# Optimization experiments

Measured on AMD Instinct MI355X. Metric: run time of the kernel, lower is better.

Reference implementation:

```python
import math
import jax, jax.numpy as jnp
import numpy as np

H = 12
D = 64  # head dim

def _heads(x):
    # [b, n, h*d] -> [b, h, n, d]
    b, n, _ = x.shape
    return x.reshape(b, n, H, D).transpose(0, 2, 1, 3)

def setup_inputs() -> dict:
    key = jax.random.key(0)
    ks = jax.random.split(key, 9)
    hs = 768
    s = 1.0 / math.sqrt(hs)
    return {
        "query_states": jax.random.normal(ks[0], (8, 1024, hs), jnp.float32),
        "key_states": jax.random.normal(ks[1], (8, 1024, hs), jnp.float32),
        "Wd": jax.random.normal(ks[2], (hs, hs), jnp.float32) * s,
        "Wq": jax.random.normal(ks[3], (hs, hs), jnp.float32) * s,
        "bq": jax.random.normal(ks[4], (hs,), jnp.float32) * 0.01,
        "Wk": jax.random.normal(ks[5], (hs, hs), jnp.float32) * s,
        "bk": jax.random.normal(ks[6], (hs,), jnp.float32) * 0.01,
        "Wv": jax.random.normal(ks[7], (hs, hs), jnp.float32) * s,
        "bv": jax.random.normal(ks[8], (hs,), jnp.float32) * 0.01,
    }

def reference(query_states, key_states, Wd, Wq, bq, Wk, bk, Wv, bv):
    # projections (torch Linear: x @ W.T + b)
    qd = _heads(query_states @ Wd.T)          # [b,h,n,d]
    kd = _heads(key_states @ Wd.T)
    q = _heads(query_states @ Wq.T + bq)
    k = _heads(key_states @ Wk.T + bk)
    v = _heads(key_states @ Wv.T + bv)
    # -0.5 * cdist(qd, kd)^2 = -0.5*(|qd|^2 + |kd|^2) + qd@kd^T
    qd_sq = jnp.sum(qd * qd, axis=-1)          # [b,h,n]
    kd_sq = jnp.sum(kd * kd, axis=-1)          # [b,h,m]
    quad = (qd @ jnp.swapaxes(kd, -1, -2)
            - 0.5 * qd_sq[..., :, None]
            - 0.5 * kd_sq[..., None, :])       # [b,h,n,m]
    lin = q @ jnp.swapaxes(k, -1, -2)          # [b,h,n,m]
    scores = (quad + lin) / math.sqrt(D)
    probs = jax.nn.softmax(scores, axis=-1)
    ctx = probs @ v                            # [b,h,n,d]
    b, _, n, _ = ctx.shape
    return ctx.transpose(0, 2, 1, 3).reshape(b, n, H * D)
```

## Files before the change

kernel.cpp:

```cpp
#include <hip/hip_runtime.h>
#include <stdint.h>

typedef __attribute__((ext_vector_type(8))) short short8;
typedef __attribute__((ext_vector_type(4))) short short4v;
typedef __attribute__((ext_vector_type(4))) float f32x4;
typedef __attribute__((ext_vector_type(16))) float f32x16;
typedef __attribute__((ext_vector_type(4))) int int4v;

static __device__ __forceinline__ unsigned short f2b(float f) {
  unsigned int u = __builtin_bit_cast(unsigned int, f);
  u += 0x7fffu + ((u >> 16) & 1u);
  return (unsigned short)(u >> 16);
}
static __device__ __forceinline__ float b2f(unsigned short b) {
  unsigned int u = ((unsigned int)b) << 16;
  return __builtin_bit_cast(float, u);
}

#define GLD16(gp, lp)                                                          \
  __builtin_amdgcn_global_load_lds(                                            \
      (const __attribute__((address_space(1))) void*)(gp),                     \
      (__attribute__((address_space(3))) void*)(lp), 16, 0, 0)

#define MFMA16 __builtin_amdgcn_mfma_f32_16x16x32_bf16
#define MFMA32 __builtin_amdgcn_mfma_f32_32x32x16_bf16

#define CVTPK(dst, lo, hi)                                                     \
  asm("v_cvt_pk_bf16_f32 %0, %1, %2" : "=v"(dst) : "v"(lo), "v"(hi))
#define PLSWAP(x, y)                                                           \
  asm volatile("v_permlane32_swap_b32 %0, %1" : "+v"(x), "+v"(y))

#define QSC 0.18033688011112113f
#define C2 0.09016844005556057f

__global__ void cvtx_kernel(const float* __restrict__ q,
                            const float* __restrict__ k,
                            unsigned short* __restrict__ Xq,
                            unsigned short* __restrict__ Xk) {
  const int bx = blockIdx.x;
  const bool lo = bx < 6144;
  const float* src = lo ? q : k;
  unsigned short* dst = lo ? Xq : Xk;
  const int i = (lo ? bx : bx - 6144) * 256 + threadIdx.x;
  float4 v = reinterpret_cast<const float4*>(src)[i];
  short4v o;
  o.x = (short)f2b(v.x);
  o.y = (short)f2b(v.y);
  o.z = (short)f2b(v.z);
  o.w = (short)f2b(v.w);
  reinterpret_cast<short4v*>(dst)[i] = o;
}

__global__ void cvtw_kernel(const float* __restrict__ Wd,
                            const float* __restrict__ Wq,
                            const float* __restrict__ Wk,
                            const float* __restrict__ Wv,
                            unsigned short* __restrict__ Wcq,
                            unsigned short* __restrict__ Wck) {
  const int bx = blockIdx.x;
  const int seg = bx / 576;
  const int i = (bx - seg * 576) * 256 + threadIdx.x;
  const float* src;
  unsigned short* dst;
  switch (seg) {
    case 0: src = Wd; dst = Wcq; break;
    case 1: src = Wq; dst = Wcq + 589824; break;
    case 2: src = Wd; dst = Wck; break;
    case 3: src = Wk; dst = Wck + 589824; break;
    default: src = Wv; dst = Wck + 1179648; break;
  }
  float4 v = reinterpret_cast<const float4*>(src)[i];
  short4v o;
  o.x = (short)f2b(v.x);
  o.y = (short)f2b(v.y);
  o.z = (short)f2b(v.z);
  o.w = (short)f2b(v.w);
  reinterpret_cast<short4v*>(dst)[i] = o;
}

__global__ __launch_bounds__(256) void proj_kernel(
    const unsigned short* __restrict__ Xq, const unsigned short* __restrict__ Xk,
    const unsigned short* __restrict__ Wcq, const unsigned short* __restrict__ Wck,
    const float* __restrict__ bq, const float* __restrict__ bk,
    const float* __restrict__ bv, unsigned short* __restrict__ Qc,
    unsigned short* __restrict__ Kc, unsigned short* __restrict__ Vt) {
  __shared__ __align__(16) short lds[2][2][128 * 32];
  const int by = blockIdx.y;
  const bool mode0 = (by < 12);
  const unsigned short* X = mode0 ? Xq : Xk;
  const unsigned short* W = mode0 ? Wcq : Wck;
  const int col0 = (mode0 ? by : by - 12) * 128;
  const int row0 = blockIdx.x * 128;
  const int lane = threadIdx.x & 63;
  const int w = threadIdx.x >> 6;
  const int wr = w >> 1, wc = w & 1;
  const int l15 = lane & 15, l4 = lane >> 4;

  f32x4 acc[4][4];
#pragma unroll
  for (int i = 0; i < 4; ++i)
#pragma unroll
    for (int j = 0; j < 4; ++j) acc[i][j] = (f32x4){0.f, 0.f, 0.f, 0.f};

  auto stage = [&](int buf, int k0) {
#pragma unroll
    for (int iss = 0; iss < 2; ++iss) {
      const int c = iss * 256 + w * 64 + lane;
      const int r = c >> 2;
      const int sl = (c & 3) ^ (r & 3);
      const unsigned short* gp = X + (size_t)(row0 + r) * 768 + k0 + sl * 8;
      GLD16(gp, (char*)&lds[buf][0][0] + (iss * 256 + w * 64) * 16);
    }
#pragma unroll
    for (int iss = 0; iss < 2; ++iss) {
      const int c = iss * 256 + w * 64 + lane;
      const int r = c >> 2;
      const int sl = (c & 3) ^ (r & 3);
      const unsigned short* gp = W + (size_t)(col0 + r) * 768 + k0 + sl * 8;
      GLD16(gp, (char*)&lds[buf][1][0] + (iss * 256 + w * 64) * 16);
    }
  };

  stage(0, 0);
  asm volatile("s_waitcnt vmcnt(0)" ::: "memory");
  __syncthreads();

  int buf = 0;
  for (int kt = 0; kt < 24; ++kt) {
    if (kt < 23) stage(buf ^ 1, (kt + 1) * 32);
    const char* Ab = (const char*)&lds[buf][0][0];
    const char* Bb = (const char*)&lds[buf][1][0];
    short8 a[4], b[4];
#pragma unroll
    for (int mt = 0; mt < 4; ++mt) {
      const int r = wr * 64 + mt * 16 + l15;
      a[mt] = *reinterpret_cast<const short8*>(Ab + r * 64 +
                                               ((l4 ^ (r & 3)) << 4));
    }
#pragma unroll
    for (int nt = 0; nt < 4; ++nt) {
      const int r = wc * 64 + nt * 16 + l15;
      b[nt] = *reinterpret_cast<const short8*>(Bb + r * 64 +
                                               ((l4 ^ (r & 3)) << 4));
    }
#pragma unroll
    for (int mt = 0; mt < 4; ++mt)
#pragma unroll
      for (int nt = 0; nt < 4; ++nt)
        acc[mt][nt] = MFMA16(a[mt], b[nt], acc[mt][nt], 0, 0, 0);
    asm volatile("s_waitcnt vmcnt(0)" ::: "memory");
    __syncthreads();
    buf ^= 1;
  }

  const int mat = mode0 ? (col0 >= 768 ? 1 : 0) : (col0 / 768);
  const int cb = col0 - mat * 768 + wc * 64;
  const float scale = mode0 ? QSC : 1.0f;
  const float* barr = mode0 ? bq : (mat == 2 ? bv : bk);
  unsigned short* outC = mode0 ? Qc : Kc;
#pragma unroll
  for (int nt = 0; nt < 4; ++nt) {
    const int cc = cb + nt * 16 + l15;
    const int hh = cc >> 6, dd = cc & 63;
    const float bias = (mat >= 1) ? barr[cc] : 0.f;
#pragma unroll
    for (int mt = 0; mt < 4; ++mt) {
#pragma unroll
      for (int i = 0; i < 4; ++i) {
        const int row = row0 + wr * 64 + mt * 16 + l4 * 4 + i;
        const int bb = row >> 10, nn = row & 1023;
        const int bhh = bb * 12 + hh;
        const float v = (acc[mt][nt][i] + bias) * scale;
        const unsigned short bvv = f2b(v);
        if (!mode0 && mat == 2)
          Vt[((size_t)bhh * 64 + dd) * 1024 + nn] = bvv;
        else
          outC[((size_t)bhh * 1024 + nn) * 128 + mat * 64 + dd] = bvv;
      }
    }
  }
}

__global__ __launch_bounds__(256) void wv_kernel(
    const unsigned short* __restrict__ Kc, unsigned short* __restrict__ wq,
    const unsigned short* __restrict__ Vt, unsigned short* __restrict__ Vs) {
  __shared__ float wf[1024];
  const int bh = blockIdx.x;
  const int t = threadIdx.x;
  const int part = t & 3;
  const unsigned short* Kb = Kc + (size_t)bh * 1024 * 128;
#pragma unroll
  for (int it = 0; it < 16; ++it) {
    const int key = it * 64 + (t >> 2);
    const short8* p =
        reinterpret_cast<const short8*>(Kb + (size_t)key * 128 + part * 16);
    float s = 0.f;
    short8 x0 = p[0], x1 = p[1];
#pragma unroll
    for (int j = 0; j < 8; ++j) {
      const float f0 = b2f((unsigned short)x0[j]);
      const float f1 = b2f((unsigned short)x1[j]);
      s += f0 * f0 + f1 * f1;
    }
    s += __shfl_xor(s, 1);
    s += __shfl_xor(s, 2);
    if (part == 0) {
      const unsigned short wb = f2b(__builtin_amdgcn_exp2f(-s * C2));
      wf[key] = b2f(wb);
      wq[(size_t)bh * 1024 + key] = wb;
    }
  }
  __syncthreads();
  const unsigned short* Vb = Vt + (size_t)bh * 64 * 1024;
  unsigned short* Ob = Vs + (size_t)bh * 64 * 1024;
#pragma unroll
  for (int i = 0; i < 32; ++i) {
    const int e0 = (i * 256 + t) * 8;
    const int k0 = e0 & 1023;
    short8 v = *reinterpret_cast<const short8*>(Vb + e0);
#pragma unroll
    for (int j = 0; j < 8; ++j)
      v[j] = (short)f2b(b2f((unsigned short)v[j]) * wf[k0 + j]);
    *reinterpret_cast<short8*>(Ob + e0) = v;
  }
}

__global__ __launch_bounds__(256, 3) void attn_kernel(
    const unsigned short* __restrict__ Qc, const unsigned short* __restrict__ Kc,
    const unsigned short* __restrict__ Vs, const unsigned short* __restrict__ wq,
    float* __restrict__ out) {
  __shared__ __align__(16) short kbuf[2][64 * 128];
  __shared__ __align__(16) short vbuf[2][64 * 64];
  __shared__ __align__(16) short wbuf[1024];

  const int bh = blockIdx.x % 96;
  const int qb = blockIdx.x / 96;
  const int b = bh / 12, h = bh - b * 12;
  const int lane = threadIdx.x & 63;
  const int w = threadIdx.x >> 6;
  const int l31 = lane & 31, l5 = lane >> 5;

  const unsigned short* Kg = Kc + (size_t)bh * 1024 * 128;
  const unsigned short* Vg = Vs + (size_t)bh * 64 * 1024;

  auto stageK = [&](int bufi, int kb) {
#pragma unroll
    for (int i = 0; i < 4; ++i) {
      const int slot = i * 256 + threadIdx.x;
      const int row = slot >> 4;
      const int d0 = ((slot & 15) ^ (row & 15)) * 8;
      const unsigned short* gp = Kg + (size_t)(kb * 64 + row) * 128 + d0;
      GLD16(gp, (char*)(&kbuf[bufi][0]) + (i * 256 + w * 64) * 16);
    }
  };
  auto stageV = [&](int bufi, int kb) {
#pragma unroll
    for (int i = 0; i < 2; ++i) {
      const int slot = i * 256 + threadIdx.x;
      const int row = slot >> 3;
      const int k0 = ((slot & 7) ^ (row & 7)) * 8;
      const unsigned short* gp = Vg + (size_t)row * 1024 + kb * 64 + k0;
      GLD16(gp, (char*)(&vbuf[bufi][0]) + (i * 256 + w * 64) * 16);
    }
  };

  stageK(0, 0);
  stageV(0, 0);
  if (w < 2) {
    const unsigned short* gp = wq + (size_t)bh * 1024 + (w * 64 + lane) * 8;
    GLD16(gp, (char*)(&wbuf[0]) + w * 1024);
  }

  const unsigned short* Qb =
      Qc + ((size_t)bh * 1024 + qb * 128 + w * 32 + l31) * 128 + l5 * 8;
  short8 qf[8];
#pragma unroll
  for (int s = 0; s < 8; ++s)
    qf[s] = *reinterpret_cast<const short8*>(Qb + s * 16);

  f32x16 o0, o1, la;
#pragma unroll
  for (int r = 0; r < 16; ++r) {
    o0[r] = 0.f;
    o1[r] = 0.f;
    la[r] = 0.f;
  }
  float m = -1e30f;

  const int S4 = (lane & 15) << 4;
  const int S3 = (lane & 7) << 4;
  const int ko = l5 * 16;

  asm volatile("s_waitcnt vmcnt(0)" ::: "memory");
  __syncthreads();

  int buf = 0;
  for (int kb = 0; kb < 16; ++kb) {
    if (kb < 15) {
      stageK(buf ^ 1, kb + 1);
      stageV(buf ^ 1, kb + 1);
    }

    const char* kB = (const char*)(&kbuf[buf][0]) + l31 * 256;
    f32x16 s0, s1;
#pragma unroll
    for (int r = 0; r < 16; ++r) {
      s0[r] = 0.f;
      s1[r] = 0.f;
    }
#pragma unroll
    for (int s = 0; s < 8; ++s) {
      const int off = (s * 32 + ko) ^ S4;
      short8 a0 = *reinterpret_cast<const short8*>(kB + off);
      short8 a1 = *reinterpret_cast<const short8*>(kB + 8192 + off);
      s0 = MFMA32(a0, qf[s], s0, 0, 0, 0);
      s1 = MFMA32(a1, qf[s], s1, 0, 0, 0);
    }

    float mx = s0[0];
#pragma unroll
    for (int r = 1; r < 16; ++r) mx = fmaxf(mx, s0[r]);
#pragma unroll
    for (int r = 0; r < 16; ++r) mx = fmaxf(mx, s1[r]);
    mx = fmaxf(mx, __shfl_xor(mx, 32));

    if (!__all(mx <= m + 11.0f)) {
      const float mn = fmaxf(m, mx);
      const float c = __builtin_amdgcn_exp2f(m - mn);
      m = mn;
      float cr[16];
#pragma unroll
      for (int r = 0; r < 16; ++r)
        cr[r] = __shfl(c, (r & 3) + 8 * (r >> 2) + 4 * l5);
#pragma unroll
      for (int r = 0; r < 16; ++r) {
        la[r] *= cr[r];
        o0[r] *= cr[r];
        o1[r] *= cr[r];
      }
    }

#pragma unroll
    for (int r = 0; r < 16; ++r) {
      s0[r] = __builtin_amdgcn_exp2f(s0[r] - m);
      s1[r] = __builtin_amdgcn_exp2f(s1[r] - m);
    }
    unsigned int u[16];
#pragma unroll
    for (int j = 0; j < 8; ++j) {
      CVTPK(u[j], s0[2 * j], s0[2 * j + 1]);
      CVTPK(u[8 + j], s1[2 * j], s1[2 * j + 1]);
    }
    PLSWAP(u[0], u[2]);
    PLSWAP(u[1], u[3]);
    PLSWAP(u[4], u[6]);
    PLSWAP(u[5], u[7]);
    PLSWAP(u[8], u[10]);
    PLSWAP(u[9], u[11]);
    PLSWAP(u[12], u[14]);
    PLSWAP(u[13], u[15]);
    short8 pa[4];
    {
      int4v t0 = {(int)u[0], (int)u[1], (int)u[2], (int)u[3]};
      int4v t1 = {(int)u[4], (int)u[5], (int)u[6], (int)u[7]};
      int4v t2 = {(int)u[8], (int)u[9], (int)u[10], (int)u[11]};
      int4v t3 = {(int)u[12], (int)u[13], (int)u[14], (int)u[15]};
      pa[0] = __builtin_bit_cast(short8, t0);
      pa[1] = __builtin_bit_cast(short8, t1);
      pa[2] = __builtin_bit_cast(short8, t2);
      pa[3] = __builtin_bit_cast(short8, t3);
    }

    const char* vB = (const char*)(&vbuf[buf][0]) + l31 * 128;
    const char* wB = (const char*)(&wbuf[0]) + kb * 128 + ko;
#pragma unroll
    for (int kk = 0; kk < 4; ++kk) {
      const int off = (kk * 32 + ko) ^ S3;
      short8 v0 = *reinterpret_cast<const short8*>(vB + off);
      short8 v1 = *reinterpret_cast<const short8*>(vB + 4096 + off);
      short8 wf = *reinterpret_cast<const short8*>(wB + kk * 32);
      o0 = MFMA32(pa[kk], v0, o0, 0, 0, 0);
      o1 = MFMA32(pa[kk], v1, o1, 0, 0, 0);
      la = MFMA32(pa[kk], wf, la, 0, 0, 0);
    }

    asm volatile("s_waitcnt vmcnt(0)" ::: "memory");
    __syncthreads();
    buf ^= 1;
  }

  const int qbase = b * 1024 + qb * 128 + w * 32;
#pragma unroll
  for (int r = 0; r < 16; ++r) {
    const float iv = __builtin_amdgcn_rcpf(la[r]);
    const int q = qbase + (r & 3) + 8 * (r >> 2) + 4 * l5;
    float* op = out + (size_t)q * 768 + h * 64 + l31;
    op[0] = o0[r] * iv;
    op[32] = o1[r] * iv;
  }
}

extern "C" void kernel_launch(void* const* d_in, const int* in_sizes, int n_in,
                              void* d_out, int out_size, void* d_ws,
                              size_t ws_size, hipStream_t stream) {
  const float* query = (const float*)d_in[0];
  const float* key = (const float*)d_in[1];
  const float* Wd = (const float*)d_in[2];
  const float* Wq = (const float*)d_in[3];
  const float* bq = (const float*)d_in[4];
  const float* Wk = (const float*)d_in[5];
  const float* bk = (const float*)d_in[6];
  const float* Wv = (const float*)d_in[7];
  const float* bv = (const float*)d_in[8];
  float* out = (float*)d_out;

  char* p = (char*)d_ws;
  auto alloc = [&](size_t n) {
    char* r = p;
    p += (n + 255) & ~(size_t)255;
    return r;
  };
  unsigned short* Xq = (unsigned short*)alloc(8192ULL * 768 * 2);
  unsigned short* Xk = (unsigned short*)alloc(8192ULL * 768 * 2);
  unsigned short* Wcq = (unsigned short*)alloc(1536ULL * 768 * 2);
  unsigned short* Wck = (unsigned short*)alloc(2304ULL * 768 * 2);
  unsigned short* Qc = (unsigned short*)alloc(96ULL * 1024 * 128 * 2);
  unsigned short* Kc = (unsigned short*)alloc(96ULL * 1024 * 128 * 2);
  unsigned short* Vt = (unsigned short*)alloc(96ULL * 64 * 1024 * 2);
  unsigned short* wqv = (unsigned short*)alloc(96ULL * 1024 * 2);
  unsigned short* Vs = Xk;

  cvtx_kernel<<<12288, 256, 0, stream>>>(query, key, Xq, Xk);
  cvtw_kernel<<<2880, 256, 0, stream>>>(Wd, Wq, Wk, Wv, Wcq, Wck);

  proj_kernel<<<dim3(64, 30), 256, 0, stream>>>(Xq, Xk, Wcq, Wck, bq, bk, bv,
                                                Qc, Kc, Vt);

  wv_kernel<<<96, 256, 0, stream>>>(Kc, wqv, Vt, Vs);

  attn_kernel<<<768, 256, 0, stream>>>(Qc, Kc, Vs, wqv, out);
}
```

Baseline: 171.1 us.

## Triple-buffer projection GEMM loads and vectorize V-transpose stores

The projection GEMM now keeps three LDS stages and waits only for the oldest group of async global-to-LDS loads (vmcnt(4)), so two tiles are in flight while the current one is consumed. A single barrier per iteration replaces the end-of-loop full drain. The epilogue for the V block now packs four consecutive sequence positions into one 8-byte store to the transposed layout instead of four scalar stores. LDS use grows by half, which may lower occupancy.

```diff
diff --git a/kernel.cpp b/kernel.cpp
--- a/kernel.cpp
+++ b/kernel.cpp
@@ -84,7 +84,7 @@
     const float* __restrict__ bq, const float* __restrict__ bk,
     const float* __restrict__ bv, unsigned short* __restrict__ Qc,
     unsigned short* __restrict__ Kc, unsigned short* __restrict__ Vt) {
-  __shared__ __align__(16) short lds[2][2][128 * 32];
+  __shared__ __align__(16) short lds[3][2][128 * 32];
   const int by = blockIdx.y;
   const bool mode0 = (by < 12);
   const unsigned short* X = mode0 ? Xq : Xk;
@@ -102,14 +102,14 @@
 #pragma unroll
     for (int j = 0; j < 4; ++j) acc[i][j] = (f32x4){0.f, 0.f, 0.f, 0.f};
 
-  auto stage = [&](int buf, int k0) {
+  auto stage = [&](int bufi, int k0) {
 #pragma unroll
     for (int iss = 0; iss < 2; ++iss) {
       const int c = iss * 256 + w * 64 + lane;
       const int r = c >> 2;
       const int sl = (c & 3) ^ (r & 3);
       const unsigned short* gp = X + (size_t)(row0 + r) * 768 + k0 + sl * 8;
-      GLD16(gp, (char*)&lds[buf][0][0] + (iss * 256 + w * 64) * 16);
+      GLD16(gp, (char*)&lds[bufi][0][0] + (iss * 256 + w * 64) * 16);
     }
 #pragma unroll
     for (int iss = 0; iss < 2; ++iss) {
@@ -117,19 +117,25 @@
       const int r = c >> 2;
       const int sl = (c & 3) ^ (r & 3);
       const unsigned short* gp = W + (size_t)(col0 + r) * 768 + k0 + sl * 8;
-      GLD16(gp, (char*)&lds[buf][1][0] + (iss * 256 + w * 64) * 16);
+      GLD16(gp, (char*)&lds[bufi][1][0] + (iss * 256 + w * 64) * 16);
     }
   };
 
   stage(0, 0);
-  asm volatile("s_waitcnt vmcnt(0)" ::: "memory");
-  __syncthreads();
-
-  int buf = 0;
+  stage(1, 32);
+
+#pragma unroll 3
   for (int kt = 0; kt < 24; ++kt) {
-    if (kt < 23) stage(buf ^ 1, (kt + 1) * 32);
-    const char* Ab = (const char*)&lds[buf][0][0];
-    const char* Bb = (const char*)&lds[buf][1][0];
+    if (kt < 23) {
+      asm volatile("s_waitcnt vmcnt(4)" ::: "memory");
+    } else {
+      asm volatile("s_waitcnt vmcnt(0)" ::: "memory");
+    }
+    __syncthreads();
+    if (kt < 22) stage((kt + 2) % 3, (kt + 2) * 32);
+
+    const char* Ab = (const char*)&lds[kt % 3][0][0];
+    const char* Bb = (const char*)&lds[kt % 3][1][0];
     short8 a[4], b[4];
 #pragma unroll
     for (int mt = 0; mt < 4; ++mt) {
@@ -148,34 +154,46 @@
 #pragma unroll
       for (int nt = 0; nt < 4; ++nt)
         acc[mt][nt] = MFMA16(a[mt], b[nt], acc[mt][nt], 0, 0, 0);
-    asm volatile("s_waitcnt vmcnt(0)" ::: "memory");
-    __syncthreads();
-    buf ^= 1;
   }
 
   const int mat = mode0 ? (col0 >= 768 ? 1 : 0) : (col0 / 768);
-  const int cb = col0 - mat * 768 + wc * 64;
-  const float scale = mode0 ? QSC : 1.0f;
+  const int cbase = col0 - mat * 768 + wc * 64;
   const float* barr = mode0 ? bq : (mat == 2 ? bv : bk);
-  unsigned short* outC = mode0 ? Qc : Kc;
-#pragma unroll
-  for (int nt = 0; nt < 4; ++nt) {
-    const int cc = cb + nt * 16 + l15;
-    const int hh = cc >> 6, dd = cc & 63;
-    const float bias = (mat >= 1) ? barr[cc] : 0.f;
-#pragma unroll
-    for (int mt = 0; mt < 4; ++mt) {
-#pragma unroll
-      for (int i = 0; i < 4; ++i) {
-        const int row = row0 + wr * 64 + mt * 16 + l4 * 4 + i;
+  if (!mode0 && mat == 2) {
+#pragma unroll
+    for (int nt = 0; nt < 4; ++nt) {
+      const int cc = cbase + nt * 16 + l15;
+      const int hh = cc >> 6, dd = cc & 63;
+      const float bias = barr[cc];
+#pragma unroll
+      for (int mt = 0; mt < 4; ++mt) {
+        const int row = row0 + wr * 64 + mt * 16 + l4 * 4;
         const int bb = row >> 10, nn = row & 1023;
-        const int bhh = bb * 12 + hh;
-        const float v = (acc[mt][nt][i] + bias) * scale;
-        const unsigned short bvv = f2b(v);
-        if (!mode0 && mat == 2)
-          Vt[((size_t)bhh * 64 + dd) * 1024 + nn] = bvv;
-        else
-          outC[((size_t)bhh * 1024 + nn) * 128 + mat * 64 + dd] = bvv;
+        short4v pv;
+#pragma unroll
+        for (int i = 0; i < 4; ++i)
+          pv[i] = (short)f2b(acc[mt][nt][i] + bias);
+        *reinterpret_cast<short4v*>(
+            Vt + ((size_t)(bb * 12 + hh) * 64 + dd) * 1024 + nn) = pv;
+      }
+    }
+  } else {
+    const float scale = mode0 ? QSC : 1.0f;
+    unsigned short* outC = mode0 ? Qc : Kc;
+#pragma unroll
+    for (int nt = 0; nt < 4; ++nt) {
+      const int cc = cbase + nt * 16 + l15;
+      const int hh = cc >> 6, dd = cc & 63;
+      const float bias = (mat >= 1) ? barr[cc] : 0.f;
+#pragma unroll
+      for (int mt = 0; mt < 4; ++mt) {
+#pragma unroll
+        for (int i = 0; i < 4; ++i) {
+          const int row = row0 + wr * 64 + mt * 16 + l4 * 4 + i;
+          const int bb = row >> 10, nn = row & 1023;
+          outC[((size_t)(bb * 12 + hh) * 1024 + nn) * 128 + mat * 64 + dd] =
+              f2b((acc[mt][nt][i] + bias) * scale);
+        }
       }
     }
   }
```

Result: faster. 164.0 us (-4.1%).
